# Optimization experiments

Measured on AMD Instinct MI355X. Metric: run time of the kernel, lower is better.

## Reference

```python
import jax, jax.numpy as jnp
import numpy as np

B, N, E = 64, 256, 8192


def setup_inputs() -> dict:
    key = jax.random.key(0)
    k1, k2, k3, k4, k5 = jax.random.split(key, 5)
    P = jax.random.uniform(k1, (B, N, N), dtype=jnp.float32)
    d_error = jax.random.uniform(k2, (N, N), dtype=jnp.float32)
    edge_i = jax.random.randint(k3, (B, E), 0, N, dtype=jnp.int32)
    edge_j = jax.random.randint(k4, (B, E), 0, N, dtype=jnp.int32)
    edge_w = jax.random.uniform(k5, (B, E), dtype=jnp.float32)
    return {"P": P, "d_error": d_error, "edge_i": edge_i,
            "edge_j": edge_j, "edge_w": edge_w}


def reference(P, d_error, edge_i, edge_j, edge_w):
    # cost_e = P[b, i_e, :] @ d_error @ P[b, j_e, :]
    # Precompute Q = P @ d_error once, then gather per edge (memory-bound).
    Q = jnp.einsum('bin,nm->bim', P, d_error)            # [B, N, N]
    Qi = jnp.take_along_axis(Q, edge_i[:, :, None], axis=1)   # [B, E, N]
    Pj = jnp.take_along_axis(P, edge_j[:, :, None], axis=1)   # [B, E, N]
    cost = jnp.sum(Qi * Pj, axis=-1)                      # [B, E]
    sample_loss = jnp.sum(edge_w * cost, axis=-1)         # [B]
    sample_weight = jnp.maximum(jnp.sum(edge_w, axis=-1), 1e-8)
    # every sample has edges -> valid_samples == B, i.e. a mean over batch
    return jnp.mean(sample_loss / sample_weight)
```

## Files before the change

### kernel.cpp

```cpp
#include <hip/hip_runtime.h>

#define NN 256
#define BB 64
#define EE 8192
#define SLD 40
#define TLD 264

typedef __attribute__((ext_vector_type(8))) short bf16x8;
typedef __attribute__((ext_vector_type(4))) float f32x4;

__device__ __forceinline__ unsigned short f2bf(float f) {
  union { float f; unsigned u; } x; x.f = f;
  unsigned r = x.u + 0x7FFFu + ((x.u >> 16) & 1u);
  return (unsigned short)(r >> 16);
}

__device__ __forceinline__ float bf2f(unsigned short h) {
  union { unsigned u; float f; } x; x.u = ((unsigned)h) << 16;
  return x.f;
}

__device__ __forceinline__ ushort4 cvt4(f32x4 v) {
  ushort4 o;
  o.x = f2bf(v[0]); o.y = f2bf(v[1]); o.z = f2bf(v[2]); o.w = f2bf(v[3]);
  return o;
}

__global__ __launch_bounds__(512, 2) void fused(const float* __restrict__ P,
                                                const float* __restrict__ D,
                                                const int* __restrict__ ei,
                                                const int* __restrict__ ej,
                                                const float* __restrict__ ew,
                                                float* __restrict__ out) {
  __shared__ __align__(16) unsigned short Stage[256 * SLD];
  __shared__ __align__(16) unsigned short BP[64 * SLD];
  __shared__ __align__(16) unsigned short Tt[64 * TLD];
  __shared__ float red[16];

  const int tid = threadIdx.x;
  const int b = blockIdx.x >> 2;
  const int jt = blockIdx.x & 3;
  const int jBase = jt * 64;

  const int lane = tid & 63;
  const int wave = tid >> 6;
  const int wm = wave * 32;
  const int frm = lane & 15;
  const int fq = (lane >> 4) * 8;
  const int crow = (lane >> 4) * 4;
  const int ccol = lane & 15;

  const float4* Pb4 = (const float4*)(P + b * NN * NN);
  const float4* D4  = (const float4*)D;

  const int srow = tid >> 3;
  const int sc4  = tid & 7;

  float4 rd[4], rp;
#pragma unroll
  for (int i = 0; i < 4; ++i) rd[i] = D4[(srow + i * 64) * 64 + sc4];
  rp = Pb4[(jBase + srow) * 64 + sc4];

  f32x4 acc[2][4];
#pragma unroll
  for (int i = 0; i < 2; ++i)
#pragma unroll
    for (int j = 0; j < 4; ++j) acc[i][j] = (f32x4){0.f, 0.f, 0.f, 0.f};

  for (int s = 0; s < 8; ++s) {
    __syncthreads();
#pragma unroll
    for (int i = 0; i < 4; ++i)
      *(ushort4*)(Stage + (srow + i * 64) * SLD + sc4 * 4) = cvt4((f32x4){rd[i].x, rd[i].y, rd[i].z, rd[i].w});
    *(ushort4*)(BP + srow * SLD + sc4 * 4) = cvt4((f32x4){rp.x, rp.y, rp.z, rp.w});
    __syncthreads();
    if (s < 7) {
      const int k4 = (s + 1) * 8;
#pragma unroll
      for (int i = 0; i < 4; ++i) rd[i] = D4[(srow + i * 64) * 64 + k4 + sc4];
      rp = Pb4[(jBase + srow) * 64 + k4 + sc4];
    } else {
#pragma unroll
      for (int i = 0; i < 4; ++i) rd[i] = Pb4[(srow + i * 64) * 64 + sc4];
    }
    bf16x8 af[2], bfr[4];
#pragma unroll
    for (int t = 0; t < 2; ++t)
      af[t] = *(const bf16x8*)(Stage + (wm + t * 16 + frm) * SLD + fq);
#pragma unroll
    for (int t = 0; t < 4; ++t)
      bfr[t] = *(const bf16x8*)(BP + (t * 16 + frm) * SLD + fq);
#pragma unroll
    for (int tr = 0; tr < 2; ++tr)
#pragma unroll
      for (int tc = 0; tc < 4; ++tc)
        acc[tr][tc] = __builtin_amdgcn_mfma_f32_16x16x32_bf16(af[tr], bfr[tc],
                                                              acc[tr][tc], 0, 0, 0);
  }

#pragma unroll
  for (int tr = 0; tr < 2; ++tr)
#pragma unroll
    for (int tc = 0; tc < 4; ++tc)
      *(ushort4*)(Tt + (tc * 16 + ccol) * TLD + wm + tr * 16 + crow) = cvt4(acc[tr][tc]);

#pragma unroll
  for (int i = 0; i < 2; ++i)
#pragma unroll
    for (int j = 0; j < 4; ++j) acc[i][j] = (f32x4){0.f, 0.f, 0.f, 0.f};

  for (int s = 0; s < 8; ++s) {
    __syncthreads();
#pragma unroll
    for (int i = 0; i < 4; ++i)
      *(ushort4*)(Stage + (srow + i * 64) * SLD + sc4 * 4) = cvt4((f32x4){rd[i].x, rd[i].y, rd[i].z, rd[i].w});
    __syncthreads();
    if (s < 7) {
      const int k4 = (s + 1) * 8;
#pragma unroll
      for (int i = 0; i < 4; ++i) rd[i] = Pb4[(srow + i * 64) * 64 + k4 + sc4];
    }
    bf16x8 af[2], bfr[4];
#pragma unroll
    for (int t = 0; t < 2; ++t)
      af[t] = *(const bf16x8*)(Stage + (wm + t * 16 + frm) * SLD + fq);
#pragma unroll
    for (int t = 0; t < 4; ++t)
      bfr[t] = *(const bf16x8*)(Tt + (t * 16 + frm) * TLD + s * 32 + fq);
#pragma unroll
    for (int tr = 0; tr < 2; ++tr)
#pragma unroll
      for (int tc = 0; tc < 4; ++tc)
        acc[tr][tc] = __builtin_amdgcn_mfma_f32_16x16x32_bf16(af[tr], bfr[tc],
                                                              acc[tr][tc], 0, 0, 0);
  }

  __syncthreads();
#pragma unroll
  for (int tr = 0; tr < 2; ++tr)
#pragma unroll
    for (int tc = 0; tc < 4; ++tc)
      *(ushort4*)(Tt + (tc * 16 + ccol) * TLD + wm + tr * 16 + crow) = cvt4(acc[tr][tc]);
  __syncthreads();

  float lsum = 0.f, wsum = 0.f;
  const int4*   ei4 = (const int4*)(ei + b * EE);
  const int4*   ej4 = (const int4*)(ej + b * EE);
  const float4* ew4 = (const float4*)(ew + b * EE);
#pragma unroll
  for (int s = 0; s < 4; ++s) {
    int idx = s * 512 + tid;
    int4 ii = ei4[idx];
    int4 jj = ej4[idx];
    float4 ww = ew4[idx];
    wsum += ww.x + ww.y + ww.z + ww.w;
    int jl;
    jl = jj.x - jBase; if ((unsigned)jl < 64u) lsum += ww.x * bf2f(Tt[jl * TLD + ii.x]);
    jl = jj.y - jBase; if ((unsigned)jl < 64u) lsum += ww.y * bf2f(Tt[jl * TLD + ii.y]);
    jl = jj.z - jBase; if ((unsigned)jl < 64u) lsum += ww.z * bf2f(Tt[jl * TLD + ii.z]);
    jl = jj.w - jBase; if ((unsigned)jl < 64u) lsum += ww.w * bf2f(Tt[jl * TLD + ii.w]);
  }
#pragma unroll
  for (int o = 32; o; o >>= 1) {
    lsum += __shfl_down(lsum, o);
    wsum += __shfl_down(wsum, o);
  }
  if (lane == 0) { red[wave] = lsum; red[8 + wave] = wsum; }
  __syncthreads();
  if (tid == 0) {
    float l = 0.f, w = 0.f;
#pragma unroll
    for (int i = 0; i < 8; ++i) { l += red[i]; w += red[8 + i]; }
    atomicAdd(out, l / (64.0f * fmaxf(w, 1e-8f)));
  }
}

extern "C" void kernel_launch(void* const* d_in, const int* in_sizes, int n_in,
                              void* d_out, int out_size, void* d_ws, size_t ws_size,
                              hipStream_t stream) {
  const float* P  = (const float*)d_in[0];
  const float* D  = (const float*)d_in[1];
  const int*   ei = (const int*)d_in[2];
  const int*   ej = (const int*)d_in[3];
  const float* ew = (const float*)d_in[4];
  float* out = (float*)d_out;

  fused<<<256, 512, 0, stream>>>(P, D, ei, ej, ew, out);
}
```

Baseline: 92.28 us.

## Double-buffer LDS staging with two-deep register prefetch and early edge loads

```diff
diff --git a/kernel.cpp b/kernel.cpp
--- a/kernel.cpp
+++ b/kernel.cpp
@@ -1,10 +1,10 @@
 #include <hip/hip_runtime.h>
 
 #define NN 256
-#define BB 64
 #define EE 8192
 #define SLD 40
 #define TLD 264
+#define SROWS 320
 
 typedef __attribute__((ext_vector_type(8))) short bf16x8;
 typedef __attribute__((ext_vector_type(4))) float f32x4;
@@ -20,9 +20,13 @@
   return x.f;
 }
 
-__device__ __forceinline__ ushort4 cvt4(f32x4 v) {
-  ushort4 o;
-  o.x = f2bf(v[0]); o.y = f2bf(v[1]); o.z = f2bf(v[2]); o.w = f2bf(v[3]);
+__device__ __forceinline__ ushort4 cvt4f(float4 v) {
+  ushort4 o; o.x = f2bf(v.x); o.y = f2bf(v.y); o.z = f2bf(v.z); o.w = f2bf(v.w);
+  return o;
+}
+
+__device__ __forceinline__ ushort4 cvt4a(f32x4 v) {
+  ushort4 o; o.x = f2bf(v[0]); o.y = f2bf(v[1]); o.z = f2bf(v[2]); o.w = f2bf(v[3]);
   return o;
 }
 
@@ -32,8 +36,7 @@
                                                 const int* __restrict__ ej,
                                                 const float* __restrict__ ew,
                                                 float* __restrict__ out) {
-  __shared__ __align__(16) unsigned short Stage[256 * SLD];
-  __shared__ __align__(16) unsigned short BP[64 * SLD];
+  __shared__ __align__(16) unsigned short Stage[2][SROWS * SLD];
   __shared__ __align__(16) unsigned short Tt[64 * TLD];
   __shared__ float red[16];
 
@@ -56,103 +59,119 @@
   const int srow = tid >> 3;
   const int sc4  = tid & 7;
 
-  float4 rd[4], rp;
-#pragma unroll
-  for (int i = 0; i < 4; ++i) rd[i] = D4[(srow + i * 64) * 64 + sc4];
-  rp = Pb4[(jBase + srow) * 64 + sc4];
-
-  f32x4 acc[2][4];
+  float4 rd[2][4];
+  float4 rp[2];
+
+  auto loadStep = [&](int g, int set) {
+    if (g < 8) {
+#pragma unroll
+      for (int i = 0; i < 4; ++i) rd[set][i] = D4[(srow + i * 64) * 64 + g * 8 + sc4];
+      rp[set] = Pb4[(jBase + srow) * 64 + g * 8 + sc4];
+    } else {
+#pragma unroll
+      for (int i = 0; i < 4; ++i) rd[set][i] = Pb4[(srow + i * 64) * 64 + (g - 8) * 8 + sc4];
+    }
+  };
+  auto writeStep = [&](int buf, int g, int set) {
+#pragma unroll
+    for (int i = 0; i < 4; ++i)
+      *(ushort4*)(&Stage[buf][(srow + i * 64) * SLD + sc4 * 4]) = cvt4f(rd[set][i]);
+    if (g < 8)
+      *(ushort4*)(&Stage[buf][(256 + srow) * SLD + sc4 * 4]) = cvt4f(rp[set]);
+  };
+
+  loadStep(0, 0);
+  loadStep(1, 1);
+  writeStep(0, 0, 0);
+  __syncthreads();
+
+  f32x4 acc1[2][4];
 #pragma unroll
   for (int i = 0; i < 2; ++i)
 #pragma unroll
-    for (int j = 0; j < 4; ++j) acc[i][j] = (f32x4){0.f, 0.f, 0.f, 0.f};
-
-  for (int s = 0; s < 8; ++s) {
+    for (int j = 0; j < 4; ++j) acc1[i][j] = (f32x4){0.f, 0.f, 0.f, 0.f};
+
+#pragma unroll
+  for (int g = 0; g < 8; ++g) {
+    const int cur = g & 1;
+    bf16x8 af[2], bfr[4];
+#pragma unroll
+    for (int t = 0; t < 2; ++t)
+      af[t] = *(const bf16x8*)(&Stage[cur][(wm + t * 16 + frm) * SLD + fq]);
+#pragma unroll
+    for (int t = 0; t < 4; ++t)
+      bfr[t] = *(const bf16x8*)(&Stage[cur][(256 + t * 16 + frm) * SLD + fq]);
+    writeStep(cur ^ 1, g + 1, (g + 1) & 1);
+    loadStep(g + 2, g & 1);
+#pragma unroll
+    for (int tr = 0; tr < 2; ++tr)
+#pragma unroll
+      for (int tc = 0; tc < 4; ++tc)
+        acc1[tr][tc] = __builtin_amdgcn_mfma_f32_16x16x32_bf16(af[tr], bfr[tc],
+                                                               acc1[tr][tc], 0, 0, 0);
+    if (g == 7) {
+#pragma unroll
+      for (int tr = 0; tr < 2; ++tr)
+#pragma unroll
+        for (int tc = 0; tc < 4; ++tc)
+          *(ushort4*)(&Tt[(tc * 16 + ccol) * TLD + wm + tr * 16 + crow]) = cvt4a(acc1[tr][tc]);
+    }
     __syncthreads();
-#pragma unroll
-    for (int i = 0; i < 4; ++i)
-      *(ushort4*)(Stage + (srow + i * 64) * SLD + sc4 * 4) = cvt4((f32x4){rd[i].x, rd[i].y, rd[i].z, rd[i].w});
-    *(ushort4*)(BP + srow * SLD + sc4 * 4) = cvt4((f32x4){rp.x, rp.y, rp.z, rp.w});
-    __syncthreads();
-    if (s < 7) {
-      const int k4 = (s + 1) * 8;
-#pragma unroll
-      for (int i = 0; i < 4; ++i) rd[i] = D4[(srow + i * 64) * 64 + k4 + sc4];
-      rp = Pb4[(jBase + srow) * 64 + k4 + sc4];
-    } else {
-#pragma unroll
-      for (int i = 0; i < 4; ++i) rd[i] = Pb4[(srow + i * 64) * 64 + sc4];
-    }
-    bf16x8 af[2], bfr[4];
-#pragma unroll
-    for (int t = 0; t < 2; ++t)
-      af[t] = *(const bf16x8*)(Stage + (wm + t * 16 + frm) * SLD + fq);
-#pragma unroll
-    for (int t = 0; t < 4; ++t)
-      bfr[t] = *(const bf16x8*)(BP + (t * 16 + frm) * SLD + fq);
-#pragma unroll
-    for (int tr = 0; tr < 2; ++tr)
-#pragma unroll
-      for (int tc = 0; tc < 4; ++tc)
-        acc[tr][tc] = __builtin_amdgcn_mfma_f32_16x16x32_bf16(af[tr], bfr[tc],
-                                                              acc[tr][tc], 0, 0, 0);
-  }
-
-#pragma unroll
-  for (int tr = 0; tr < 2; ++tr)
-#pragma unroll
-    for (int tc = 0; tc < 4; ++tc)
-      *(ushort4*)(Tt + (tc * 16 + ccol) * TLD + wm + tr * 16 + crow) = cvt4(acc[tr][tc]);
-
-#pragma unroll
-  for (int i = 0; i < 2; ++i)
-#pragma unroll
-    for (int j = 0; j < 4; ++j) acc[i][j] = (f32x4){0.f, 0.f, 0.f, 0.f};
-
-  for (int s = 0; s < 8; ++s) {
-    __syncthreads();
-#pragma unroll
-    for (int i = 0; i < 4; ++i)
-      *(ushort4*)(Stage + (srow + i * 64) * SLD + sc4 * 4) = cvt4((f32x4){rd[i].x, rd[i].y, rd[i].z, rd[i].w});
-    __syncthreads();
-    if (s < 7) {
-      const int k4 = (s + 1) * 8;
-#pragma unroll
-      for (int i = 0; i < 4; ++i) rd[i] = Pb4[(srow + i * 64) * 64 + k4 + sc4];
-    }
-    bf16x8 af[2], bfr[4];
-#pragma unroll
-    for (int t = 0; t < 2; ++t)
-      af[t] = *(const bf16x8*)(Stage + (wm + t * 16 + frm) * SLD + fq);
-#pragma unroll
-    for (int t = 0; t < 4; ++t)
-      bfr[t] = *(const bf16x8*)(Tt + (t * 16 + frm) * TLD + s * 32 + fq);
-#pragma unroll
-    for (int tr = 0; tr < 2; ++tr)
-#pragma unroll
-      for (int tc = 0; tc < 4; ++tc)
-        acc[tr][tc] = __builtin_amdgcn_mfma_f32_16x16x32_bf16(af[tr], bfr[tc],
-                                                              acc[tr][tc], 0, 0, 0);
-  }
-
-  __syncthreads();
-#pragma unroll
-  for (int tr = 0; tr < 2; ++tr)
-#pragma unroll
-    for (int tc = 0; tc < 4; ++tc)
-      *(ushort4*)(Tt + (tc * 16 + ccol) * TLD + wm + tr * 16 + crow) = cvt4(acc[tr][tc]);
-  __syncthreads();
-
-  float lsum = 0.f, wsum = 0.f;
+  }
+
   const int4*   ei4 = (const int4*)(ei + b * EE);
   const int4*   ej4 = (const int4*)(ej + b * EE);
   const float4* ew4 = (const float4*)(ew + b * EE);
+  int4 eii[4], ejj[4];
+  float4 eww[4];
 #pragma unroll
   for (int s = 0; s < 4; ++s) {
-    int idx = s * 512 + tid;
-    int4 ii = ei4[idx];
-    int4 jj = ej4[idx];
-    float4 ww = ew4[idx];
+    eii[s] = ei4[s * 512 + tid];
+    ejj[s] = ej4[s * 512 + tid];
+    eww[s] = ew4[s * 512 + tid];
+  }
+
+  f32x4 acc2[2][4];
+#pragma unroll
+  for (int i = 0; i < 2; ++i)
+#pragma unroll
+    for (int j = 0; j < 4; ++j) acc2[i][j] = (f32x4){0.f, 0.f, 0.f, 0.f};
+
+#pragma unroll
+  for (int g2 = 0; g2 < 8; ++g2) {
+    const int g = 8 + g2;
+    const int cur = g & 1;
+    bf16x8 af[2], bfr[4];
+#pragma unroll
+    for (int t = 0; t < 2; ++t)
+      af[t] = *(const bf16x8*)(&Stage[cur][(wm + t * 16 + frm) * SLD + fq]);
+#pragma unroll
+    for (int t = 0; t < 4; ++t)
+      bfr[t] = *(const bf16x8*)(&Tt[(t * 16 + frm) * TLD + g2 * 32 + fq]);
+    if (g2 < 7) writeStep(cur ^ 1, g + 1, (g + 1) & 1);
+    if (g2 < 6) loadStep(g + 2, g & 1);
+#pragma unroll
+    for (int tr = 0; tr < 2; ++tr)
+#pragma unroll
+      for (int tc = 0; tc < 4; ++tc)
+        acc2[tr][tc] = __builtin_amdgcn_mfma_f32_16x16x32_bf16(af[tr], bfr[tc],
+                                                               acc2[tr][tc], 0, 0, 0);
+    __syncthreads();
+  }
+
+#pragma unroll
+  for (int tr = 0; tr < 2; ++tr)
+#pragma unroll
+    for (int tc = 0; tc < 4; ++tc)
+      *(ushort4*)(&Tt[(tc * 16 + ccol) * TLD + wm + tr * 16 + crow]) = cvt4a(acc2[tr][tc]);
+  __syncthreads();
+
+  float lsum = 0.f, wsum = 0.f;
+#pragma unroll
+  for (int s = 0; s < 4; ++s) {
+    int4 ii = eii[s];
+    int4 jj = ejj[s];
+    float4 ww = eww[s];
     wsum += ww.x + ww.y + ww.z + ww.w;
     int jl;
     jl = jj.x - jBase; if ((unsigned)jl < 64u) lsum += ww.x * bf2f(Tt[jl * TLD + ii.x]);
```

New measurement: 88.36 us. 1.04x faster.

## Load MFMA operands directly from global into registers, dropping LDS staging

Applied to the files above, without the earlier changes.

```diff
diff --git a/kernel.cpp b/kernel.cpp
--- a/kernel.cpp
+++ b/kernel.cpp
@@ -1,29 +1,33 @@
 #include <hip/hip_runtime.h>
+#include <hip/hip_bf16.h>
 
 #define NN 256
-#define BB 64
 #define EE 8192
-#define SLD 40
 #define TLD 264
 
 typedef __attribute__((ext_vector_type(8))) short bf16x8;
 typedef __attribute__((ext_vector_type(4))) float f32x4;
-
-__device__ __forceinline__ unsigned short f2bf(float f) {
-  union { float f; unsigned u; } x; x.f = f;
-  unsigned r = x.u + 0x7FFFu + ((x.u >> 16) & 1u);
-  return (unsigned short)(r >> 16);
-}
 
 __device__ __forceinline__ float bf2f(unsigned short h) {
   union { unsigned u; float f; } x; x.u = ((unsigned)h) << 16;
   return x.f;
 }
 
-__device__ __forceinline__ ushort4 cvt4(f32x4 v) {
-  ushort4 o;
-  o.x = f2bf(v[0]); o.y = f2bf(v[1]); o.z = f2bf(v[2]); o.w = f2bf(v[3]);
-  return o;
+__device__ __forceinline__ unsigned pack2(float x, float y) {
+  union { __hip_bfloat162 h; unsigned u; } c;
+  c.h = __float22bfloat162_rn(make_float2(x, y));
+  return c.u;
+}
+__device__ __forceinline__ bf16x8 cvt8(float4 a, float4 b) {
+  union { bf16x8 v; unsigned u[4]; } r;
+  r.u[0] = pack2(a.x, a.y); r.u[1] = pack2(a.z, a.w);
+  r.u[2] = pack2(b.x, b.y); r.u[3] = pack2(b.z, b.w);
+  return r.v;
+}
+__device__ __forceinline__ ushort4 cvt4a(f32x4 v) {
+  union { ushort4 s; unsigned u[2]; } r;
+  r.u[0] = pack2(v[0], v[1]); r.u[1] = pack2(v[2], v[3]);
+  return r.s;
 }
 
 __global__ __launch_bounds__(512, 2) void fused(const float* __restrict__ P,
@@ -32,8 +36,6 @@
                                                 const int* __restrict__ ej,
                                                 const float* __restrict__ ew,
                                                 float* __restrict__ out) {
-  __shared__ __align__(16) unsigned short Stage[256 * SLD];
-  __shared__ __align__(16) unsigned short BP[64 * SLD];
   __shared__ __align__(16) unsigned short Tt[64 * TLD];
   __shared__ float red[16];
 
@@ -47,19 +49,24 @@
   const int wm = wave * 32;
   const int frm = lane & 15;
   const int fq = (lane >> 4) * 8;
+  const int fq4 = fq >> 2;
   const int crow = (lane >> 4) * 4;
   const int ccol = lane & 15;
 
   const float4* Pb4 = (const float4*)(P + b * NN * NN);
   const float4* D4  = (const float4*)D;
 
-  const int srow = tid >> 3;
-  const int sc4  = tid & 7;
+  const float4* aRow0 = D4 + (wm + frm) * 64;
+  const float4* aRow1 = D4 + (wm + 16 + frm) * 64;
+  const float4* bRow[4];
+#pragma unroll
+  for (int t = 0; t < 4; ++t) bRow[t] = Pb4 + (jBase + t * 16 + frm) * 64;
 
-  float4 rd[4], rp;
+  float4 la[2][2], lb[4][2];
+  la[0][0] = aRow0[fq4]; la[0][1] = aRow0[fq4 + 1];
+  la[1][0] = aRow1[fq4]; la[1][1] = aRow1[fq4 + 1];
 #pragma unroll
-  for (int i = 0; i < 4; ++i) rd[i] = D4[(srow + i * 64) * 64 + sc4];
-  rp = Pb4[(jBase + srow) * 64 + sc4];
+  for (int t = 0; t < 4; ++t) { lb[t][0] = bRow[t][fq4]; lb[t][1] = bRow[t][fq4 + 1]; }
 
   f32x4 acc[2][4];
 #pragma unroll
@@ -67,29 +74,20 @@
 #pragma unroll
     for (int j = 0; j < 4; ++j) acc[i][j] = (f32x4){0.f, 0.f, 0.f, 0.f};
 
-  for (int s = 0; s < 8; ++s) {
-    __syncthreads();
 #pragma unroll
-    for (int i = 0; i < 4; ++i)
-      *(ushort4*)(Stage + (srow + i * 64) * SLD + sc4 * 4) = cvt4((f32x4){rd[i].x, rd[i].y, rd[i].z, rd[i].w});
-    *(ushort4*)(BP + srow * SLD + sc4 * 4) = cvt4((f32x4){rp.x, rp.y, rp.z, rp.w});
-    __syncthreads();
-    if (s < 7) {
-      const int k4 = (s + 1) * 8;
+  for (int g = 0; g < 8; ++g) {
+    bf16x8 af[2], bfr[4];
+    af[0] = cvt8(la[0][0], la[0][1]);
+    af[1] = cvt8(la[1][0], la[1][1]);
 #pragma unroll
-      for (int i = 0; i < 4; ++i) rd[i] = D4[(srow + i * 64) * 64 + k4 + sc4];
-      rp = Pb4[(jBase + srow) * 64 + k4 + sc4];
-    } else {
+    for (int t = 0; t < 4; ++t) bfr[t] = cvt8(lb[t][0], lb[t][1]);
+    if (g < 7) {
+      const int off = (g + 1) * 8 + fq4;
+      la[0][0] = aRow0[off]; la[0][1] = aRow0[off + 1];
+      la[1][0] = aRow1[off]; la[1][1] = aRow1[off + 1];
 #pragma unroll
-      for (int i = 0; i < 4; ++i) rd[i] = Pb4[(srow + i * 64) * 64 + sc4];
+      for (int t = 0; t < 4; ++t) { lb[t][0] = bRow[t][off]; lb[t][1] = bRow[t][off + 1]; }
     }
-    bf16x8 af[2], bfr[4];
-#pragma unroll
-    for (int t = 0; t < 2; ++t)
-      af[t] = *(const bf16x8*)(Stage + (wm + t * 16 + frm) * SLD + fq);
-#pragma unroll
-    for (int t = 0; t < 4; ++t)
-      bfr[t] = *(const bf16x8*)(BP + (t * 16 + frm) * SLD + fq);
 #pragma unroll
     for (int tr = 0; tr < 2; ++tr)
 #pragma unroll
@@ -102,31 +100,44 @@
   for (int tr = 0; tr < 2; ++tr)
 #pragma unroll
     for (int tc = 0; tc < 4; ++tc)
-      *(ushort4*)(Tt + (tc * 16 + ccol) * TLD + wm + tr * 16 + crow) = cvt4(acc[tr][tc]);
+      *(ushort4*)(&Tt[(tc * 16 + ccol) * TLD + wm + tr * 16 + crow]) = cvt4a(acc[tr][tc]);
+  __syncthreads();
+
+  const float4* pRow0 = Pb4 + (wm + frm) * 64;
+  const float4* pRow1 = Pb4 + (wm + 16 + frm) * 64;
+  la[0][0] = pRow0[fq4]; la[0][1] = pRow0[fq4 + 1];
+  la[1][0] = pRow1[fq4]; la[1][1] = pRow1[fq4 + 1];
+
+  const int4*   ei4 = (const int4*)(ei + b * EE);
+  const int4*   ej4 = (const int4*)(ej + b * EE);
+  const float4* ew4 = (const float4*)(ew + b * EE);
+  int4 eii[4], ejj[4];
+  float4 eww[4];
+#pragma unroll
+  for (int s = 0; s < 4; ++s) {
+    eii[s] = ei4[s * 512 + tid];
+    ejj[s] = ej4[s * 512 + tid];
+    eww[s] = ew4[s * 512 + tid];
+  }
 
 #pragma unroll
   for (int i = 0; i < 2; ++i)
 #pragma unroll
     for (int j = 0; j < 4; ++j) acc[i][j] = (f32x4){0.f, 0.f, 0.f, 0.f};
 
-  for (int s = 0; s < 8; ++s) {
-    __syncthreads();
 #pragma unroll
-    for (int i = 0; i < 4; ++i)
-      *(ushort4*)(Stage + (srow + i * 64) * SLD + sc4 * 4) = cvt4((f32x4){rd[i].x, rd[i].y, rd[i].z, rd[i].w});
-    __syncthreads();
-    if (s < 7) {
-      const int k4 = (s + 1) * 8;
-#pragma unroll
-      for (int i = 0; i < 4; ++i) rd[i] = Pb4[(srow + i * 64) * 64 + k4 + sc4];
-    }
+  for (int g = 0; g < 8; ++g) {
     bf16x8 af[2], bfr[4];
-#pragma unroll
-    for (int t = 0; t < 2; ++t)
-      af[t] = *(const bf16x8*)(Stage + (wm + t * 16 + frm) * SLD + fq);
+    af[0] = cvt8(la[0][0], la[0][1]);
+    af[1] = cvt8(la[1][0], la[1][1]);
 #pragma unroll
     for (int t = 0; t < 4; ++t)
-      bfr[t] = *(const bf16x8*)(Tt + (t * 16 + frm) * TLD + s * 32 + fq);
+      bfr[t] = *(const bf16x8*)(&Tt[(t * 16 + frm) * TLD + g * 32 + fq]);
+    if (g < 7) {
+      const int off = (g + 1) * 8 + fq4;
+      la[0][0] = pRow0[off]; la[0][1] = pRow0[off + 1];
+      la[1][0] = pRow1[off]; la[1][1] = pRow1[off + 1];
+    }
 #pragma unroll
     for (int tr = 0; tr < 2; ++tr)
 #pragma unroll
@@ -140,19 +151,15 @@
   for (int tr = 0; tr < 2; ++tr)
 #pragma unroll
     for (int tc = 0; tc < 4; ++tc)
-      *(ushort4*)(Tt + (tc * 16 + ccol) * TLD + wm + tr * 16 + crow) = cvt4(acc[tr][tc]);
+      *(ushort4*)(&Tt[(tc * 16 + ccol) * TLD + wm + tr * 16 + crow]) = cvt4a(acc[tr][tc]);
   __syncthreads();
 
   float lsum = 0.f, wsum = 0.f;
-  const int4*   ei4 = (const int4*)(ei + b * EE);
-  const int4*   ej4 = (const int4*)(ej + b * EE);
-  const float4* ew4 = (const float4*)(ew + b * EE);
 #pragma unroll
   for (int s = 0; s < 4; ++s) {
-    int idx = s * 512 + tid;
-    int4 ii = ei4[idx];
-    int4 jj = ej4[idx];
-    float4 ww = ew4[idx];
+    int4 ii = eii[s];
+    int4 jj = ejj[s];
+    float4 ww = eww[s];
     wsum += ww.x + ww.y + ww.z + ww.w;
     int jl;
     jl = jj.x - jBase; if ((unsigned)jl < 64u) lsum += ww.x * bf2f(Tt[jl * TLD + ii.x]);
```

Measured after the change: 105.7 us. 1.15x slower.
